# Performance work log

Measured on AMD Instinct MI355X. Metric: run time of the kernel, lower is better.

## Reference

```python
import jax, jax.numpy as jnp
import numpy as np

N_TOTAL_BINS = 15  # torch.linspace(0, 1, 15 + 1) hardcodes 15 bins


def setup_inputs() -> dict:
    key = jax.random.key(0)
    k1, k2, k3, k4 = jax.random.split(key, 4)
    n, c, h, w = 8, 21, 513, 513
    predict = jax.random.normal(k1, (n, c, h, w), dtype=jnp.float32)
    target = jax.random.randint(k2, (n, h, w), 0, c, dtype=jnp.int64)
    confidence = jax.random.uniform(k3, (n * h * w,), dtype=jnp.float32)
    accuracies = jax.random.uniform(k4, (N_TOTAL_BINS,), dtype=jnp.float32)
    return {
        "predict": predict,
        "target": target,
        "confidence": confidence,
        "accuracies": accuracies,
        "n_bin": 15,
    }


def reference(predict, target, confidence, accuracies, n_bin):
    n, c, h, w = predict.shape
    # NCHW -> NHWC -> [N*H*W, C], log_softmax over classes, gather target logp
    logits = predict.transpose(0, 2, 3, 1).reshape(-1, c)
    logp = jax.nn.log_softmax(logits, axis=-1)
    logp_t = jnp.take_along_axis(logp, target.reshape(-1, 1), axis=1)[:, 0]  # [N*H*W]

    # Single-pass binning: bin i covers (i/15, (i+1)/15], last used bin's upper
    # boundary is forced to 1 (bin_uppers[-1] = 1), hence the clip to n_bin-1.
    bin_id = jnp.clip(
        jnp.ceil(confidence * N_TOTAL_BINS).astype(jnp.int32) - 1, 0, n_bin - 1
    )
    valid = (confidence > 0.0) & (confidence <= 1.0)

    acc = accuracies[:n_bin]
    coeff_bin = acc * 10.0 - (1.0 - acc) * 50.0          # per-bin coefficient
    pos_bin = coeff_bin > 0.0                            # only coeff > 0 bins count

    sel = valid & pos_bin[bin_id]
    per_coeff = jnp.where(sel, coeff_bin[bin_id], 0.0)
    size = jnp.sum(sel.astype(jnp.float32))
    calibrated_loss = -jnp.sum(logp_t * per_coeff) / size
    return calibrated_loss
```

## Files before the change

### kernel.cpp

```cpp
#include <hip/hip_runtime.h>

#define N_IMG   8
#define C_CH    21
#define HW      263169
#define P_TOT   (N_IMG * HW)
#define NBINS   15
#define QPI     65793
#define NQ      (N_IMG * QPI)
#define BLOCKS  2057

typedef float f4u __attribute__((ext_vector_type(4), aligned(4)));
typedef int   i4u __attribute__((ext_vector_type(4), aligned(4)));


__global__ __launch_bounds__(256) void cce2d_main(
    const float* __restrict__ predict,
    const int*   __restrict__ target,
    const float* __restrict__ conf,
    const float* __restrict__ acc,
    const int*   __restrict__ n_bin_p,
    double*      __restrict__ ws_sum,
    unsigned int* __restrict__ ws_cnt)
{
    const int qid_raw = blockIdx.x * blockDim.x + threadIdx.x;
    const int qid  = min(qid_raw, NQ - 1);
    const int n    = qid / QPI;
    const int q    = qid - n * QPI;
    const int lo   = 4 * q;
    const int rem0 = min(lo, HW - 4);

    const float* base = predict + (size_t)n * (size_t)(C_CH * HW) + (size_t)rem0;
    const int p0 = n * HW + rem0;

    const f4u cf4 = *(const f4u*)(conf + p0);
    const i4u tg4 = *(const i4u*)(target + p0);

    float s [4] = {0.f, 0.f, 0.f, 0.f};
    float xt[4] = {0.f, 0.f, 0.f, 0.f};

    #pragma unroll
    for (int c = 0; c < C_CH; ++c) {
        const f4u x = *(const f4u*)(base + (size_t)c * HW);
        #pragma unroll
        for (int j = 0; j < 4; ++j) {
            s[j] += __expf(x[j]);
            xt[j] = (c == tg4[j]) ? x[j] : xt[j];
        }
    }

    const int n_bin = n_bin_p[0];
    float contrib = 0.0f;
    unsigned int cnt = 0;
    #pragma unroll
    for (int j = 0; j < 4; ++j) {
        const bool cover = (qid_raw < NQ) && (rem0 + j >= lo);
        const float cf = cf4[j];
        const bool valid = (cf > 0.0f) && (cf <= 1.0f);
        int bin = (int)ceilf(cf * (float)NBINS) - 1;
        bin = min(max(bin, 0), n_bin - 1);
        const float a  = acc[bin];
        const float co = a * 10.0f - (1.0f - a) * 50.0f;
        const bool sel = valid && (co > 0.0f) && cover;
        contrib += sel ? (xt[j] - __logf(s[j])) * co : 0.0f;
        cnt     += sel ? 1u : 0u;
    }

    #pragma unroll
    for (int off = 32; off > 0; off >>= 1) {
        contrib += __shfl_down(contrib, off);
        cnt     += __shfl_down(cnt, off);
    }

    __shared__ float        s_v[4];
    __shared__ unsigned int s_c[4];
    const int lane = threadIdx.x & 63;
    const int wid  = threadIdx.x >> 6;
    if (lane == 0) { s_v[wid] = contrib; s_c[wid] = cnt; }
    __syncthreads();

    if (threadIdx.x == 0) {
        const float v = s_v[0] + s_v[1] + s_v[2] + s_v[3];
        const unsigned int cc = s_c[0] + s_c[1] + s_c[2] + s_c[3];
        atomicAdd(ws_sum, (double)v);
        atomicAdd(ws_cnt, cc);
    }
}

__global__ void cce2d_final(const double* __restrict__ ws_sum,
                            const unsigned int* __restrict__ ws_cnt,
                            float* __restrict__ out)
{
    const unsigned int c = *ws_cnt;
    const double s = *ws_sum;
    out[0] = (float)(-s / (double)(c ? c : 1u));
}

extern "C" void kernel_launch(void* const* d_in, const int* in_sizes, int n_in,
                              void* d_out, int out_size, void* d_ws, size_t ws_size,
                              hipStream_t stream) {
    const float* predict = (const float*)d_in[0];
    const int*   target  = (const int*)  d_in[1];
    const float* conf    = (const float*)d_in[2];
    const float* acc     = (const float*)d_in[3];
    const int*   n_bin_p = (const int*)  d_in[4];

    double*       ws_sum = (double*)d_ws;
    unsigned int* ws_cnt = (unsigned int*)((char*)d_ws + 8);

    hipMemsetAsync(d_ws, 0, 16, stream);

    cce2d_main<<<BLOCKS, 256, 0, stream>>>(predict, target, conf, acc, n_bin_p,
                                           ws_sum, ws_cnt);
    cce2d_final<<<1, 1, 0, stream>>>(ws_sum, ws_cnt, (float*)d_out);
}
```

Before: 269.8 us.

## Use grid-stride loop with batched nontemporal loads over fewer blocks

Replaces the one-quad-per-thread launch of 2057 blocks with a 512-block grid-stride loop in which each thread handles up to five quads. All 21 channel vectors are loaded up front with nontemporal loads, launch bounds request two blocks per SM, and the number of per-block atomics drops. The aim is more memory-level parallelism and less block scheduling and atomic overhead for this bandwidth-bound reduction. The risks are higher register pressure from holding 84 floats per quad and lower occupancy, which could hurt latency hiding.

```diff
diff --git a/kernel.cpp b/kernel.cpp
--- a/kernel.cpp
+++ b/kernel.cpp
@@ -7,53 +7,48 @@
 #define NBINS   15
 #define QPI     65793
 #define NQ      (N_IMG * QPI)
-#define BLOCKS  2057
+#define BLOCKS  512
+#define TSTRIDE (BLOCKS * 256)
+#define FULL_IT 4
 
 typedef float f4u __attribute__((ext_vector_type(4), aligned(4)));
 typedef int   i4u __attribute__((ext_vector_type(4), aligned(4)));
 
 
-__global__ __launch_bounds__(256) void cce2d_main(
-    const float* __restrict__ predict,
-    const int*   __restrict__ target,
-    const float* __restrict__ conf,
-    const float* __restrict__ acc,
-    const int*   __restrict__ n_bin_p,
-    double*      __restrict__ ws_sum,
-    unsigned int* __restrict__ ws_cnt)
+__device__ __forceinline__ void do_quad(int qid,
+    const float* __restrict__ predict, const int* __restrict__ target,
+    const float* __restrict__ conf,    const float* __restrict__ acc,
+    int n_bin, float& contrib, unsigned int& cnt)
 {
-    const int qid_raw = blockIdx.x * blockDim.x + threadIdx.x;
-    const int qid  = min(qid_raw, NQ - 1);
     const int n    = qid / QPI;
     const int q    = qid - n * QPI;
     const int lo   = 4 * q;
     const int rem0 = min(lo, HW - 4);
-
     const float* base = predict + (size_t)n * (size_t)(C_CH * HW) + (size_t)rem0;
     const int p0 = n * HW + rem0;
 
     const f4u cf4 = *(const f4u*)(conf + p0);
     const i4u tg4 = *(const i4u*)(target + p0);
 
-    float s [4] = {0.f, 0.f, 0.f, 0.f};
+    f4u x[C_CH];
+    #pragma unroll
+    for (int c = 0; c < C_CH; ++c)
+        x[c] = __builtin_nontemporal_load((const f4u*)(base + (size_t)c * HW));
+
+    float s[4]  = {0.f, 0.f, 0.f, 0.f};
     float xt[4] = {0.f, 0.f, 0.f, 0.f};
-
     #pragma unroll
     for (int c = 0; c < C_CH; ++c) {
-        const f4u x = *(const f4u*)(base + (size_t)c * HW);
         #pragma unroll
         for (int j = 0; j < 4; ++j) {
-            s[j] += __expf(x[j]);
-            xt[j] = (c == tg4[j]) ? x[j] : xt[j];
+            s[j] += __expf(x[c][j]);
+            xt[j] = (c == tg4[j]) ? x[c][j] : xt[j];
         }
     }
 
-    const int n_bin = n_bin_p[0];
-    float contrib = 0.0f;
-    unsigned int cnt = 0;
     #pragma unroll
     for (int j = 0; j < 4; ++j) {
-        const bool cover = (qid_raw < NQ) && (rem0 + j >= lo);
+        const bool cover = (rem0 + j >= lo);
         const float cf = cf4[j];
         const bool valid = (cf > 0.0f) && (cf <= 1.0f);
         int bin = (int)ceilf(cf * (float)NBINS) - 1;
@@ -64,6 +59,30 @@
         contrib += sel ? (xt[j] - __logf(s[j])) * co : 0.0f;
         cnt     += sel ? 1u : 0u;
     }
+}
+
+__global__ __launch_bounds__(256, 2) void cce2d_main(
+    const float* __restrict__ predict,
+    const int*   __restrict__ target,
+    const float* __restrict__ conf,
+    const float* __restrict__ acc,
+    const int*   __restrict__ n_bin_p,
+    double*      __restrict__ ws_sum,
+    unsigned int* __restrict__ ws_cnt)
+{
+    const int tid   = blockIdx.x * blockDim.x + threadIdx.x;
+    const int n_bin = n_bin_p[0];
+
+    float contrib = 0.0f;
+    unsigned int cnt = 0;
+
+    #pragma unroll
+    for (int i = 0; i < FULL_IT; ++i)
+        do_quad(tid + i * TSTRIDE, predict, target, conf, acc, n_bin, contrib, cnt);
+
+    const int q4 = tid + FULL_IT * TSTRIDE;
+    if (q4 < NQ)
+        do_quad(q4, predict, target, conf, acc, n_bin, contrib, cnt);
 
     #pragma unroll
     for (int off = 32; off > 0; off >>= 1) {
```

After: 288.5 us. 1.07x slower.
